# Kernel tuning notes

Hardware: AMD Instinct MI355X
Metric: run time of the kernel (lower is better)

Reference implementation:

```python
import jax, jax.numpy as jnp
import numpy as np

L, D, A = 3, 128, 64
NREL2 = 2 * 200 + 1
N_NODE, N_EDGE = 100000, 600000
NQ, N_ENT = 512, 50000


def setup_inputs() -> dict:
    key = jax.random.key(0)
    ks = jax.random.split(key, 30)
    s = 0.05
    inp = {
        "rela_embed": jax.random.normal(ks[0], (L, NREL2, D)) * s,
        "Ws": jax.random.normal(ks[1], (L, A, D)) * s,
        "Wr": jax.random.normal(ks[2], (L, A, D)) * s,
        "Wqr_w": jax.random.normal(ks[3], (L, A, D)) * s,
        "Wqr_b": jax.random.normal(ks[4], (L, A)) * s,
        "Wtau": jax.random.normal(ks[5], (L, A, D)) * s,
        "walpha_w": jax.random.normal(ks[6], (L, 1, A)) * s,
        "walpha_b": jax.random.normal(ks[7], (L, 1)) * s,
        "Wh": jax.random.normal(ks[8], (L, D, D)) * s,
        "wt1": jax.random.normal(ks[9], (L, 1, D)) * s,
        "bt1": jax.random.normal(ks[10], (L, 1, D)) * s,
        "wt2": jax.random.normal(ks[11], (L, 1, D)) * s,
        "bt2": jax.random.normal(ks[12], (L, 1, D)) * s,
        "Wih": jax.random.normal(ks[13], (L, 3 * D, D)) * s,
        "Whh": jax.random.normal(ks[14], (L, 3 * D, D)) * s,
        "bih": jax.random.normal(ks[15], (L, 3 * D)) * s,
        "bhh": jax.random.normal(ks[16], (L, 3 * D)) * s,
        "Wfinal": jax.random.normal(ks[17], (D,)) * s,
        "q_rel": jax.random.randint(ks[18], (NQ,), 0, NREL2),
        "q_tau": jax.random.randint(ks[19], (NQ,), 0, 366),
        "edge_ridx": jax.random.randint(ks[20], (L, N_EDGE), 0, NQ),
        "edge_rel": jax.random.randint(ks[21], (L, N_EDGE), 0, NREL2),
        "edge_tau": jax.random.randint(ks[22], (L, N_EDGE), 0, 366),
        "edge_sub": jax.random.randint(ks[23], (L, N_EDGE), 0, N_NODE),
        "edge_obj": jax.random.randint(ks[24], (L, N_EDGE), 0, N_NODE),
        "nodes_batch": jax.random.randint(ks[25], (N_NODE,), 0, NQ),
        "nodes_ent": jax.random.randint(ks[26], (N_NODE,), 0, N_ENT),
        "n_ent": N_ENT,
    }
    return inp


def _gru_cell(x, h, Wih, Whh, bih, bhh):
    # PyTorch GRU cell semantics (seq_len == 1)
    gi = x @ Wih.T + bih  # [N, 3D]
    gh = h @ Whh.T + bhh
    i_r, i_z, i_n = jnp.split(gi, 3, axis=-1)
    h_r, h_z, h_n = jnp.split(gh, 3, axis=-1)
    r = jax.nn.sigmoid(i_r + h_r)
    z = jax.nn.sigmoid(i_z + h_z)
    n = jnp.tanh(i_n + r * h_n)
    return (1.0 - z) * n + z * h


def reference(rela_embed, Ws, Wr, Wqr_w, Wqr_b, Wtau, walpha_w, walpha_b, Wh,
              wt1, bt1, wt2, bt2, Wih, Whh, bih, bhh, Wfinal,
              q_rel, q_tau, edge_ridx, edge_rel, edge_tau, edge_sub, edge_obj,
              nodes_batch, nodes_ent, n_ent):
    n_node = nodes_batch.shape[0]
    nq = q_rel.shape[0]
    d = Wh.shape[-1]
    hidden = jnp.zeros((n_node, d), dtype=rela_embed.dtype)
    h0 = jnp.zeros((n_node, d), dtype=rela_embed.dtype)
    coe_timediff = 0.2  # computed in original but unused downstream

    for l in range(rela_embed.shape[0]):
        sub, rel, obj = edge_sub[l], edge_rel[l], edge_obj[l]
        ridx = edge_ridx[l]
        hs = hidden[sub]                      # [E, D] gather
        hr = rela_embed[l][rel]               # [E, D] embedding gather
        h_qr = rela_embed[l][q_rel][ridx]     # [E, D]
        taus_q = q_tau[ridx]
        tau = jnp.where(edge_tau[l] >= 0, edge_tau[l], taus_q)
        delta = (tau - taus_q).astype(rela_embed.dtype)[:, None]  # [E, 1]
        h_hau = wt1[l] * delta + bt1[l] + jnp.sin(wt2[l] * delta + bt2[l])
        message = hs + hr + h_hau
        attn = jax.nn.relu(hs @ Ws[l].T + hr @ Wr[l].T + h_qr @ Wqr_w[l].T
                           + Wqr_b[l] + h_hau @ Wtau[l].T)  # [E, A]
        alpha = jax.nn.sigmoid(attn @ walpha_w[l].T + walpha_b[l])  # [E, 1]
        msg = alpha * message
        agg = jax.ops.segment_sum(msg, obj, num_segments=n_node)  # scatter-add
        hidden = jax.nn.relu(agg @ Wh[l].T)
        # old_nodes_new_idx == identity here, so index_copy of h0 is passthrough
        h = _gru_cell(hidden, h0, Wih[l], Whh[l], bih[l], bhh[l])
        hidden, h0 = h, h

    scores = hidden @ Wfinal  # [n_node]
    scores_all = jnp.zeros((nq, n_ent), dtype=scores.dtype)
    scores_all = scores_all.at[nodes_batch, nodes_ent].set(scores)
    return scores_all
```

## Files before the change

kernel.cpp:

```cpp
#include <hip/hip_runtime.h>
#include <hip/hip_bf16.h>
#include <math.h>

typedef __hip_bfloat16 bf16;
typedef __attribute__((ext_vector_type(8))) short s8v;
typedef __attribute__((ext_vector_type(4))) float f4v;
typedef __attribute__((ext_vector_type(4))) float f4x;
typedef __attribute__((ext_vector_type(4))) short s4v;

constexpr int Lc = 3, Dc = 128, Ac = 64, NREL2c = 401;
constexpr int NEc = 600000, NNc = 100000, NQc = 512, NENTc = 50000;
constexpr int NTAUc = 731;
constexpr int HBITS = 18;
constexpr unsigned HSIZE = 1u << HBITS, HMASK = HSIZE - 1u;
constexpr int NBLK = (NNc + 255) / 256;
constexpr int NTILE = 4;

constexpr float SFX = 32767.f, SFXI = 1.f / 32767.f;

constexpr int O_RELA = 0;
constexpr int O_WS   = O_RELA + Lc * NREL2c * Dc;
constexpr int O_WR   = O_WS   + Lc * Ac * Dc;
constexpr int O_WQRW = O_WR   + Lc * Ac * Dc;
constexpr int O_WQRB = O_WQRW + Lc * Ac * Dc;
constexpr int O_WTAU = O_WQRB + Lc * Ac;
constexpr int O_WAW  = O_WTAU + Lc * Ac * Dc;
constexpr int O_WAB  = O_WAW  + Lc * Ac;
constexpr int O_WH   = O_WAB  + Lc;
constexpr int O_WT1  = O_WH   + Lc * Dc * Dc;
constexpr int O_BT1  = O_WT1  + Lc * Dc;
constexpr int O_WT2  = O_BT1  + Lc * Dc;
constexpr int O_BT2  = O_WT2  + Lc * Dc;
constexpr int O_WIH  = O_BT2  + Lc * Dc;
constexpr int O_WHH  = O_WIH  + Lc * 3 * Dc * Dc;
constexpr int O_BIH  = O_WHH  + Lc * 3 * Dc * Dc;
constexpr int O_BHH  = O_BIH  + Lc * 3 * Dc;
constexpr int O_WF   = O_BHH  + Lc * 3 * Dc;
constexpr int NWTAB  = O_WF + Dc;

__device__ const int KOFF[19] = {O_RELA, O_WS, O_WR, O_WQRW, O_WQRB, O_WTAU, O_WAW,
                                 O_WAB, O_WH, O_WT1, O_BT1, O_WT2, O_BT2, O_WIH,
                                 O_WHH, O_BIH, O_BHH, O_WF, NWTAB};

struct Ptrs { const void* p[18]; };

__device__ __forceinline__ float b2f(bf16 x) { return __bfloat162float(x); }
__device__ __forceinline__ float bsf(unsigned short u) {
  return __uint_as_float((unsigned)u << 16);
}
__device__ __forceinline__ float sigm(float x) { return 1.f / (1.f + expf(-x)); }
__device__ __forceinline__ float s2f(short s) { return (float)s * SFXI; }
__device__ __forceinline__ short f2s(float v) { return (short)__float2int_rn(v * SFX); }
__device__ __forceinline__ unsigned short f2b(float v) {
  bf16 h = __float2bfloat16(v);
  return *(unsigned short*)&h;
}
__device__ __forceinline__ f4v mfma16(s8v a, s8v b, f4v c) {
  return __builtin_amdgcn_mfma_f32_16x16x32_bf16(a, b, c, 0, 0, 0);
}

__global__ void detect_dtype(const unsigned* __restrict__ w, int* __restrict__ flag) {
  int lane = threadIdx.x & 63;
  int cnt = 0;
  for (int k = lane; k < 256; k += 64) {
    unsigned e = (w[k] >> 7) & 0xffu;
    cnt += (e >= 96u && e <= 140u) ? 1 : 0;
  }
#pragma unroll
  for (int o = 32; o; o >>= 1) cnt += __shfl_xor(cnt, o, 64);
  if (lane == 0) *flag = (cnt >= 128) ? 0 : 1;
}

__global__ void convert_weights(Ptrs ps, const int* __restrict__ flag,
                                unsigned short* __restrict__ wtab) {
  int idx = blockIdx.x * 256 + threadIdx.x;
  if (idx >= NWTAB) return;
  int b = 0;
  while (idx >= KOFF[b + 1]) ++b;
  int j = idx - KOFF[b];
  unsigned short v;
  if (*flag) v = f2b(((const float*)ps.p[b])[j]);
  else v = ((const unsigned short*)ps.p[b])[j];
  wtab[idx] = v;
}

__global__ void prep_hhau(int l, const bf16* __restrict__ W, float* __restrict__ Hh) {
  int idx = blockIdx.x * 256 + threadIdx.x;
  if (idx >= NTAUc * Dc) return;
  int t = idx >> 7, d = idx & 127;
  float delta = (float)(t - 365);
  Hh[idx] = b2f(W[O_WT1 + l * Dc + d]) * delta + b2f(W[O_BT1 + l * Dc + d]) +
            sinf(b2f(W[O_WT2 + l * Dc + d]) * delta + b2f(W[O_BT2 + l * Dc + d]));
}

__global__ void prep_yr(int l, const bf16* __restrict__ W, float* __restrict__ Yr) {
  int idx = blockIdx.x * 256 + threadIdx.x;
  if (idx >= NREL2c * Ac) return;
  int r = idx >> 6, a = idx & 63;
  const bf16* x = W + O_RELA + (size_t)(l * NREL2c + r) * Dc;
  const bf16* w = W + O_WR + (size_t)(l * Ac + a) * Dc;
  float s = 0.f;
  for (int d = 0; d < Dc; ++d) s = fmaf(b2f(x[d]), b2f(w[d]), s);
  Yr[idx] = s;
}

__global__ void prep_yqr(int l, const bf16* __restrict__ W, const int* __restrict__ q_rel,
                         float* __restrict__ Yqr) {
  int idx = blockIdx.x * 256 + threadIdx.x;
  if (idx >= NQc * Ac) return;
  int q = idx >> 6, a = idx & 63;
  const bf16* x = W + O_RELA + (size_t)(l * NREL2c + q_rel[q]) * Dc;
  const bf16* w = W + O_WQRW + (size_t)(l * Ac + a) * Dc;
  float s = b2f(W[O_WQRB + l * Ac + a]);
  for (int d = 0; d < Dc; ++d) s = fmaf(b2f(x[d]), b2f(w[d]), s);
  Yqr[idx] = s;
}

__global__ void prep_yh(int l, const float* __restrict__ Hh, const bf16* __restrict__ W,
                        float* __restrict__ Yh) {
  int idx = blockIdx.x * 256 + threadIdx.x;
  if (idx >= NTAUc * Ac) return;
  int t = idx >> 6, a = idx & 63;
  const float* x = Hh + (size_t)t * Dc;
  const bf16* w = W + O_WTAU + (size_t)(l * Ac + a) * Dc;
  float s = 0.f;
  for (int d = 0; d < Dc; ++d) s = fmaf(x[d], b2f(w[d]), s);
  Yh[idx] = s;
}

__global__ void k_count(const int* __restrict__ e_obj, int base, int* __restrict__ cnt) {
  int e = blockIdx.x * 256 + threadIdx.x;
  if (e < NEc) atomicAdd(&cnt[e_obj[base + e]], 1);
}

__global__ void k_scan1(const int* __restrict__ cnt, int* __restrict__ bsum) {
  __shared__ int s[256];
  int t = threadIdx.x, g = blockIdx.x * 256 + t;
  s[t] = g < NNc ? cnt[g] : 0;
  __syncthreads();
  for (int o = 128; o > 0; o >>= 1) {
    if (t < o) s[t] += s[t + o];
    __syncthreads();
  }
  if (t == 0) bsum[blockIdx.x] = s[0];
}

__global__ void k_scan2(const int* __restrict__ bsum, int* __restrict__ bpre,
                        int* __restrict__ offsets) {
  if (threadIdx.x == 0) {
    int run = 0;
    for (int i = 0; i < NBLK; ++i) { bpre[i] = run; run += bsum[i]; }
    offsets[NNc] = run;
  }
}

__global__ void k_scan3(const int* __restrict__ cnt, const int* __restrict__ bpre,
                        int* __restrict__ offsets, int* __restrict__ cursor) {
  __shared__ int s[256];
  int t = threadIdx.x, g = blockIdx.x * 256 + t;
  int c = g < NNc ? cnt[g] : 0;
  s[t] = c;
  __syncthreads();
  for (int o = 1; o < 256; o <<= 1) {
    int v = (t >= o) ? s[t - o] : 0;
    __syncthreads();
    s[t] += v;
    __syncthreads();
  }
  if (g < NNc) {
    int off = s[t] - c + bpre[blockIdx.x];
    offsets[g] = off;
    cursor[g] = off;
  }
}

__global__ void k_fill(const int* __restrict__ e_obj, int base, int* __restrict__ cursor,
                       int* __restrict__ eidx) {
  int e = blockIdx.x * 256 + threadIdx.x;
  if (e < NEc) {
    int pos = atomicAdd(&cursor[e_obj[base + e]], 1);
    eidx[pos] = e;
  }
}

__global__ __launch_bounds__(256, 2) void alpha_kernel(
    int l, const bf16* __restrict__ W, const int* __restrict__ e_sub,
    const int* __restrict__ e_rel, const int* __restrict__ e_ridx,
    const int* __restrict__ e_tau, const int* __restrict__ q_tau,
    const short* __restrict__ state, const float* __restrict__ Yr,
    const float* __restrict__ Yqr, const float* __restrict__ Yh,
    float* __restrict__ alphab, unsigned short* __restrict__ dixb) {
  const int tid = threadIdx.x, lane = tid & 63, w = tid >> 6;
  const int col = lane & 15, quad = lane >> 4;
  const unsigned short* Wu = (const unsigned short*)W;
  s8v Bf[4][4];
  if (l != 0) {
#pragma unroll
    for (int kt = 0; kt < 4; ++kt)
#pragma unroll
      for (int ct = 0; ct < 4; ++ct)
        Bf[kt][ct] =
            *(const s8v*)&Wu[O_WS + (size_t)(l * Ac + ct * 16 + col) * Dc + kt * 32 + quad * 8];
  }
  float wa[4];
#pragma unroll
  for (int ct = 0; ct < 4; ++ct) wa[ct] = b2f(W[O_WAW + l * Ac + ct * 16 + col]);
  const float wb = b2f(W[O_WAB + l]);
  const int base = l * NEc;
  const int gw0 = blockIdx.x * 4 + w, nw = gridDim.x * 4;
  for (int g = gw0; g < NEc / 16; g += nw) {
    int e0 = g * 16;
    int sub16 = e_sub[base + e0 + col];
    int rel16 = e_rel[base + e0 + col];
    int ridx16 = e_ridx[base + e0 + col];
    int et16 = e_tau[base + e0 + col];
    int tq16 = q_tau[ridx16];
    int dix16 = ((et16 >= 0) ? et16 : tq16) - tq16 + 365;
    if (lane < 16) dixb[e0 + lane] = (unsigned short)dix16;
    f4v acc[4];
#pragma unroll
    for (int ct = 0; ct < 4; ++ct) acc[ct] = (f4v)0.f;
    if (l != 0) {
#pragma unroll
      for (int kt = 0; kt < 4; ++kt) {
        const short* sp = &state[(size_t)sub16 * Dc + kt * 32 + quad * 8];
        s8v raw = *(const s8v*)sp;
        s8v a;
#pragma unroll
        for (int j = 0; j < 8; ++j) a[j] = (short)f2b((float)raw[j] * SFXI);
#pragma unroll
        for (int ct = 0; ct < 4; ++ct) acc[ct] = mfma16(a, Bf[kt][ct], acc[ct]);
      }
    }
    float sums[4];
#pragma unroll
    for (int r = 0; r < 4; ++r) {
      int m = quad * 4 + r;
      int rel_m = __shfl(rel16, m, 64);
      int ridx_m = __shfl(ridx16, m, 64);
      int dix_m = __shfl(dix16, m, 64);
      float s = 0.f;
#pragma unroll
      for (int ct = 0; ct < 4; ++ct) {
        int a = ct * 16 + col;
        float v = acc[ct][r] + Yr[rel_m * Ac + a] + Yqr[ridx_m * Ac + a] + Yh[dix_m * Ac + a];
        s = fmaf(fmaxf(v, 0.f), wa[ct], s);
      }
      s += __shfl_xor(s, 1, 64);
      s += __shfl_xor(s, 2, 64);
      s += __shfl_xor(s, 4, 64);
      s += __shfl_xor(s, 8, 64);
      sums[r] = s;
    }
    int rr = col - quad * 4;
    if (rr >= 0 && rr < 4) alphab[e0 + col] = sigm(sums[rr] + wb);
  }
}

__global__ __launch_bounds__(256) void gather_kernel(
    int l, const bf16* __restrict__ W, const int* __restrict__ offsets,
    const int* __restrict__ eidx, const float* __restrict__ alphab,
    const unsigned short* __restrict__ dixb, const int* __restrict__ e_sub,
    const int* __restrict__ e_rel, const short* __restrict__ state,
    const float* __restrict__ Hh, float* __restrict__ agg) {
  const int lane = threadIdx.x & 63;
  const int gw = (blockIdx.x * 256 + threadIdx.x) >> 6;
  const int nw = (gridDim.x * 256) >> 6;
  const int base = l * NEc;
  for (int i = gw; i < NNc; i += nw) {
    float a0 = 0.f, a1 = 0.f;
    int s = offsets[i], en = offsets[i + 1];
    for (int p = s; p < en; ++p) {
      int e = eidx[p];
      float al = alphab[e];
      int rel = e_rel[base + e];
      int dix = dixb[e];
      float hs0 = 0.f, hs1 = 0.f;
      if (l != 0) {
        int sub = e_sub[base + e];
        hs0 = s2f(state[(size_t)sub * Dc + lane]);
        hs1 = s2f(state[(size_t)sub * Dc + 64 + lane]);
      }
      const bf16* hrp = W + O_RELA + (size_t)(l * NREL2c + rel) * Dc;
      a0 = fmaf(al, hs0 + b2f(hrp[lane]) + Hh[dix * Dc + lane], a0);
      a1 = fmaf(al, hs1 + b2f(hrp[64 + lane]) + Hh[dix * Dc + 64 + lane], a1);
    }
    agg[(size_t)i * Dc + lane] = a0;
    agg[(size_t)i * Dc + 64 + lane] = a1;
  }
}

__global__ __launch_bounds__(256, 2) void node_update(
    int l, const bf16* __restrict__ W, const float* __restrict__ agg,
    short* __restrict__ state) {
  __shared__ __align__(16) unsigned short ldsAhi[64][136];
  __shared__ __align__(16) unsigned short ldsAlo[64][136];
  __shared__ __align__(16) unsigned short ldsH[64][136];
  const int tid = threadIdx.x;
  const int lane = tid & 63;
  const int w = tid >> 6;
  const int col = lane & 15;
  const int quad = lane >> 4;
  const int kb = quad * 8;
  const unsigned short* Wu = (const unsigned short*)W;

  s8v whb[2][4];
#pragma unroll
  for (int kt = 0; kt < 4; ++kt) {
    whb[0][kt] = *(const s8v*)&Wu[O_WH + (size_t)(l * Dc + w * 16 + col) * Dc + kt * 32 + kb];
    whb[1][kt] =
        *(const s8v*)&Wu[O_WH + (size_t)(l * Dc + (w + 4) * 16 + col) * Dc + kt * 32 + kb];
  }

#pragma unroll 1
  for (int tile = 0; tile < NTILE; ++tile) {
    const int n0 = (blockIdx.x * NTILE + tile) * 64;
    if (n0 >= NNc) break;
    if (tile) __syncthreads();
    for (int e = tid; e < 64 * 32; e += 256) {
      int i = e >> 5, c = (e & 31) * 4;
      int node = n0 + i;
      f4x av = (f4x)0.f;
      if (node < NNc) av = __builtin_nontemporal_load((const f4x*)&agg[(size_t)node * Dc + c]);
      s4v hi4, lo4;
#pragma unroll
      for (int j = 0; j < 4; ++j) {
        unsigned short hi = f2b(av[j]);
        hi4[j] = (short)hi;
        lo4[j] = (short)f2b(av[j] - bsf(hi));
      }
      *(s4v*)&ldsAhi[i][c] = hi4;
      *(s4v*)&ldsAlo[i][c] = lo4;
      if (l != 0) {
        s4v hv4 = (s4v)0, hb4;
        if (node < NNc) hv4 = *(const s4v*)&state[(size_t)node * Dc + c];
#pragma unroll
        for (int j = 0; j < 4; ++j) hb4[j] = (short)f2b(s2f(hv4[j]));
        *(s4v*)&ldsH[i][c] = hb4;
      }
    }
    __syncthreads();

    f4v xo[2][4];
#pragma unroll
    for (int c = 0; c < 2; ++c)
#pragma unroll
      for (int mt = 0; mt < 4; ++mt) xo[c][mt] = (f4v)0.f;
#pragma unroll
    for (int kt = 0; kt < 4; ++kt) {
      int ko = kt * 32 + kb;
#pragma unroll
      for (int mt = 0; mt < 4; ++mt) {
        s8v ahi = *(const s8v*)&ldsAhi[mt * 16 + col][ko];
        s8v alo = *(const s8v*)&ldsAlo[mt * 16 + col][ko];
        xo[0][mt] = mfma16(ahi, whb[0][kt], xo[0][mt]);
        xo[0][mt] = mfma16(alo, whb[0][kt], xo[0][mt]);
        xo[1][mt] = mfma16(ahi, whb[1][kt], xo[1][mt]);
        xo[1][mt] = mfma16(alo, whb[1][kt], xo[1][mt]);
      }
    }
    __syncthreads();
#pragma unroll
    for (int c = 0; c < 2; ++c) {
      int t = w + 4 * c;
#pragma unroll
      for (int mt = 0; mt < 4; ++mt) {
#pragma unroll
        for (int r = 0; r < 4; ++r) {
          float x = fmaxf(xo[c][mt][r], 0.f);
          unsigned short hi = f2b(x);
          ldsAhi[mt * 16 + quad * 4 + r][t * 16 + col] = hi;
          ldsAlo[mt * 16 + quad * 4 + r][t * 16 + col] = f2b(x - bsf(hi));
        }
      }
    }
    __syncthreads();

#pragma unroll 1
    for (int hs = 0; hs < 2; ++hs) {
      const int jcol = hs * 64 + w * 16 + col;
      const int R = l * 384 + jcol;
      f4v racc[4], zacc[4], niacc[4], nhacc[4];
#pragma unroll
      for (int mt = 0; mt < 4; ++mt) {
        racc[mt] = (f4v)0.f;
        zacc[mt] = (f4v)0.f;
        niacc[mt] = (f4v)0.f;
        nhacc[mt] = (f4v)0.f;
      }
#pragma unroll
      for (int kt = 0; kt < 4; ++kt) {
        int ko = kt * 32 + kb;
        s8v bir = *(const s8v*)&Wu[O_WIH + (size_t)R * Dc + ko];
        s8v biz = *(const s8v*)&Wu[O_WIH + (size_t)(R + 128) * Dc + ko];
        s8v bin = *(const s8v*)&Wu[O_WIH + (size_t)(R + 256) * Dc + ko];
#pragma unroll
        for (int mt = 0; mt < 4; ++mt) {
          s8v xhi = *(const s8v*)&ldsAhi[mt * 16 + col][ko];
          s8v xlo = *(const s8v*)&ldsAlo[mt * 16 + col][ko];
          racc[mt] = mfma16(xhi, bir, racc[mt]);
          racc[mt] = mfma16(xlo, bir, racc[mt]);
          zacc[mt] = mfma16(xhi, biz, zacc[mt]);
          zacc[mt] = mfma16(xlo, biz, zacc[mt]);
          niacc[mt] = mfma16(xhi, bin, niacc[mt]);
          niacc[mt] = mfma16(xlo, bin, niacc[mt]);
        }
        if (l != 0) {
          s8v bhr = *(const s8v*)&Wu[O_WHH + (size_t)R * Dc + ko];
          s8v bhz = *(const s8v*)&Wu[O_WHH + (size_t)(R + 128) * Dc + ko];
          s8v bhn = *(const s8v*)&Wu[O_WHH + (size_t)(R + 256) * Dc + ko];
#pragma unroll
          for (int mt = 0; mt < 4; ++mt) {
            s8v hf = *(const s8v*)&ldsH[mt * 16 + col][ko];
            racc[mt] = mfma16(hf, bhr, racc[mt]);
            zacc[mt] = mfma16(hf, bhz, zacc[mt]);
            nhacc[mt] = mfma16(hf, bhn, nhacc[mt]);
          }
        }
      }
      float bir_ = b2f(W[O_BIH + R]) + b2f(W[O_BHH + R]);
      float biz_ = b2f(W[O_BIH + R + 128]) + b2f(W[O_BHH + R + 128]);
      float bin_ = b2f(W[O_BIH + R + 256]);
      float bhn_ = b2f(W[O_BHH + R + 256]);
#pragma unroll
      for (int mt = 0; mt < 4; ++mt) {
#pragma unroll
        for (int r_ = 0; r_ < 4; ++r_) {
          int node = n0 + mt * 16 + quad * 4 + r_;
          if (node < NNc) {
            float rg = sigm(racc[mt][r_] + bir_);
            float zg = sigm(zacc[mt][r_] + biz_);
            float ng = tanhf(niacc[mt][r_] + bin_ + rg * (nhacc[mt][r_] + bhn_));
            size_t idx = (size_t)node * Dc + jcol;
            float h0 = (l != 0) ? s2f(state[idx]) : 0.f;
            __builtin_nontemporal_store(f2s((1.f - zg) * ng + zg * h0), &state[idx]);
          }
        }
      }
    }
  }
}

__global__ __launch_bounds__(256) void score_kernel(const short* __restrict__ state,
                                                    const bf16* __restrict__ W,
                                                    float* __restrict__ scores) {
  const int lane = threadIdx.x & 63;
  const int gw = (blockIdx.x * 256 + threadIdx.x) >> 6;
  const int nw = (gridDim.x * 256) >> 6;
  const float w0 = b2f(W[O_WF + lane]), w1 = b2f(W[O_WF + 64 + lane]);
  for (int i = gw; i < NNc; i += nw) {
    float v = s2f(state[(size_t)i * Dc + lane]) * w0 + s2f(state[(size_t)i * Dc + 64 + lane]) * w1;
#pragma unroll
    for (int o = 32; o; o >>= 1) v += __shfl_xor(v, o, 64);
    if (lane == 0) scores[i] = v;
  }
}

__global__ void zero_out(unsigned* __restrict__ out, const int* __restrict__ flag) {
  long words = ((long)NQc * NENTc / 2) * (*flag ? 2 : 1);
  long i = (long)blockIdx.x * 256 + threadIdx.x;
  long stride = (long)gridDim.x * 256;
  for (; i < words; i += stride) out[i] = 0u;
}

__device__ __forceinline__ unsigned hpos(unsigned pos) { return (pos * 2654435761u) >> (32 - HBITS); }

__global__ void scat1(const int* __restrict__ nb, const int* __restrict__ ne,
                      unsigned* __restrict__ hkey, int* __restrict__ hval) {
  int i = blockIdx.x * 256 + threadIdx.x;
  if (i >= NNc) return;
  unsigned pos = (unsigned)(nb[i] * NENTc + ne[i]);
  unsigned key = pos + 1u;
  unsigned h = hpos(pos);
  while (true) {
    unsigned prev = atomicCAS(&hkey[h], 0u, key);
    if (prev == 0u || prev == key) {
      atomicMax(&hval[h], i);
      break;
    }
    h = (h + 1u) & HMASK;
  }
}

__global__ void scat2(const int* __restrict__ nb, const int* __restrict__ ne,
                      const unsigned* __restrict__ hkey, const int* __restrict__ hval,
                      const float* __restrict__ scores, const int* __restrict__ flag,
                      void* __restrict__ out) {
  int i = blockIdx.x * 256 + threadIdx.x;
  if (i >= NNc) return;
  unsigned pos = (unsigned)(nb[i] * NENTc + ne[i]);
  unsigned key = pos + 1u;
  unsigned h = hpos(pos);
  while (true) {
    unsigned k = hkey[h];
    if (k == key) {
      if (hval[h] == i) {
        if (*flag) ((float*)out)[pos] = scores[i];
        else ((bf16*)out)[pos] = __float2bfloat16(scores[i]);
      }
      break;
    }
    if (k == 0u) break;
    h = (h + 1u) & HMASK;
  }
}

extern "C" void kernel_launch(void* const* d_in, const int* in_sizes, int n_in,
                              void* d_out, int out_size, void* d_ws, size_t ws_size,
                              hipStream_t stream) {
  const int* q_rel = (const int*)d_in[18];
  const int* q_tau = (const int*)d_in[19];
  const int* e_ridx = (const int*)d_in[20];
  const int* e_rel = (const int*)d_in[21];
  const int* e_tau = (const int*)d_in[22];
  const int* e_sub = (const int*)d_in[23];
  const int* e_obj = (const int*)d_in[24];
  const int* n_batch = (const int*)d_in[25];
  const int* n_ent_i = (const int*)d_in[26];

  char* p = (char*)d_ws;
  auto alloc = [&](size_t bytes) {
    void* r = (void*)p;
    p += (bytes + 255) & ~(size_t)255;
    return r;
  };
  int* flag = (int*)alloc(256);
  bf16* wtab = (bf16*)alloc((size_t)NWTAB * 2);
  short* state = (short*)alloc((size_t)NNc * Dc * 2);
  char* big = (char*)alloc((size_t)NNc * Dc * 2);
  float* Yr = (float*)big;
  float* Yqr = (float*)(big + 102912);
  float* Hh = (float*)(big + 233984);
  float* Yh = (float*)(big + 608256);
  float* alphab = (float*)(big + 800000);
  unsigned short* dixb = (unsigned short*)(big + 3200000);
  int* cnt = (int*)(big + 4400128);
  int* cursor = (int*)(big + 4800384);
  int* offsets = (int*)(big + 5200640);
  int* bsum = (int*)(big + 5600768);
  int* bpre = (int*)(big + 5602560);
  int* eidx = (int*)(big + 5604352);
  float* scores = (float*)big;
  unsigned* hkey = (unsigned*)(big + 400128);
  int* hval = (int*)(big + 400128 + (size_t)HSIZE * 4);

  float* agg = (float*)d_out;

  detect_dtype<<<1, 64, 0, stream>>>((const unsigned*)d_in[0], flag);
  Ptrs ps;
  for (int i = 0; i < 18; ++i) ps.p[i] = d_in[i];
  convert_weights<<<(NWTAB + 255) / 256, 256, 0, stream>>>(ps, flag, (unsigned short*)wtab);
  hipMemsetAsync(state, 0, (size_t)NNc * Dc * 2, stream);

  for (int l = 0; l < Lc; ++l) {
    hipMemsetAsync(cnt, 0, (size_t)NNc * 4, stream);
    prep_hhau<<<(NTAUc * Dc + 255) / 256, 256, 0, stream>>>(l, wtab, Hh);
    prep_yr<<<(NREL2c * Ac + 255) / 256, 256, 0, stream>>>(l, wtab, Yr);
    prep_yqr<<<(NQc * Ac + 255) / 256, 256, 0, stream>>>(l, wtab, q_rel, Yqr);
    prep_yh<<<(NTAUc * Ac + 255) / 256, 256, 0, stream>>>(l, Hh, wtab, Yh);
    k_count<<<(NEc + 255) / 256, 256, 0, stream>>>(e_obj, l * NEc, cnt);
    k_scan1<<<NBLK, 256, 0, stream>>>(cnt, bsum);
    k_scan2<<<1, 64, 0, stream>>>(bsum, bpre, offsets);
    k_scan3<<<NBLK, 256, 0, stream>>>(cnt, bpre, offsets, cursor);
    k_fill<<<(NEc + 255) / 256, 256, 0, stream>>>(e_obj, l * NEc, cursor, eidx);
    alpha_kernel<<<2048, 256, 0, stream>>>(l, wtab, e_sub, e_rel, e_ridx, e_tau, q_tau,
                                           state, Yr, Yqr, Yh, alphab, dixb);
    gather_kernel<<<2048, 256, 0, stream>>>(l, wtab, offsets, eidx, alphab, dixb, e_sub,
                                            e_rel, state, Hh, agg);
    node_update<<<(NNc + 64 * NTILE - 1) / (64 * NTILE), 256, 0, stream>>>(l, wtab, agg, state);
  }
  score_kernel<<<1024, 256, 0, stream>>>(state, wtab, scores);
  hipMemsetAsync(hkey, 0, (size_t)HSIZE * 4, stream);
  hipMemsetAsync(hval, 0, (size_t)HSIZE * 4, stream);
  zero_out<<<2048, 256, 0, stream>>>((unsigned*)d_out, flag);
  scat1<<<(NNc + 255) / 256, 256, 0, stream>>>(n_batch, n_ent_i, hkey, hval);
  scat2<<<(NNc + 255) / 256, 256, 0, stream>>>(n_batch, n_ent_i, hkey, hval, scores, flag, d_out);
}
```

Baseline: 1.892 ms.

## Stage GRU outputs in LDS for coalesced state writes and reuse cached h0

The GRU gate computation moves into a templated helper that returns results in registers. Outputs are staged through LDS and written to state as 16-byte coalesced rows, replacing scattered 2-byte nontemporal stores and the per-element global re-read of h0, which now comes from the raw fixed-point copy in LDS. Occupancy is raised to 3 blocks per SM and NTILE is halved. The costs are an extra conversion of the fixed-point h into bf16 inside the inner MFMA loop, two more barriers per tile, and higher register pressure under the tighter launch bound.

```diff
diff --git a/kernel.cpp b/kernel.cpp
--- a/kernel.cpp
+++ b/kernel.cpp
@@ -14,7 +14,7 @@
 constexpr int HBITS = 18;
 constexpr unsigned HSIZE = 1u << HBITS, HMASK = HSIZE - 1u;
 constexpr int NBLK = (NNc + 255) / 256;
-constexpr int NTILE = 4;
+constexpr int NTILE = 2;
 
 constexpr float SFX = 32767.f, SFXI = 1.f / 32767.f;
 
@@ -290,7 +290,73 @@
   }
 }
 
-__global__ __launch_bounds__(256, 2) void node_update(
+template <int HS>
+__device__ __forceinline__ void gate_half(
+    int l, const unsigned short* __restrict__ Wu, const bf16* __restrict__ W,
+    int w, int col, int quad, int kb, int n0,
+    unsigned short (&ldsAhi)[64][136], unsigned short (&ldsAlo)[64][136],
+    unsigned short (&ldsH)[64][136], float (&hout)[16]) {
+  const int jcol = HS * 64 + w * 16 + col;
+  const int R = l * 384 + jcol;
+  f4v racc[4], zacc[4], niacc[4], nhacc[4];
+#pragma unroll
+  for (int mt = 0; mt < 4; ++mt) {
+    racc[mt] = (f4v)0.f;
+    zacc[mt] = (f4v)0.f;
+    niacc[mt] = (f4v)0.f;
+    nhacc[mt] = (f4v)0.f;
+  }
+#pragma unroll
+  for (int kt = 0; kt < 4; ++kt) {
+    int ko = kt * 32 + kb;
+    s8v bir = *(const s8v*)&Wu[O_WIH + (size_t)R * Dc + ko];
+    s8v biz = *(const s8v*)&Wu[O_WIH + (size_t)(R + 128) * Dc + ko];
+    s8v bin = *(const s8v*)&Wu[O_WIH + (size_t)(R + 256) * Dc + ko];
+#pragma unroll
+    for (int mt = 0; mt < 4; ++mt) {
+      s8v xhi = *(const s8v*)&ldsAhi[mt * 16 + col][ko];
+      s8v xlo = *(const s8v*)&ldsAlo[mt * 16 + col][ko];
+      racc[mt] = mfma16(xhi, bir, racc[mt]);
+      racc[mt] = mfma16(xlo, bir, racc[mt]);
+      zacc[mt] = mfma16(xhi, biz, zacc[mt]);
+      zacc[mt] = mfma16(xlo, biz, zacc[mt]);
+      niacc[mt] = mfma16(xhi, bin, niacc[mt]);
+      niacc[mt] = mfma16(xlo, bin, niacc[mt]);
+    }
+    if (l != 0) {
+      s8v bhr = *(const s8v*)&Wu[O_WHH + (size_t)R * Dc + ko];
+      s8v bhz = *(const s8v*)&Wu[O_WHH + (size_t)(R + 128) * Dc + ko];
+      s8v bhn = *(const s8v*)&Wu[O_WHH + (size_t)(R + 256) * Dc + ko];
+#pragma unroll
+      for (int mt = 0; mt < 4; ++mt) {
+        s8v raw = *(const s8v*)&ldsH[mt * 16 + col][ko];
+        s8v hf;
+#pragma unroll
+        for (int j = 0; j < 8; ++j) hf[j] = (short)f2b((float)raw[j] * SFXI);
+        racc[mt] = mfma16(hf, bhr, racc[mt]);
+        zacc[mt] = mfma16(hf, bhz, zacc[mt]);
+        nhacc[mt] = mfma16(hf, bhn, nhacc[mt]);
+      }
+    }
+  }
+  float bir_ = b2f(W[O_BIH + R]) + b2f(W[O_BHH + R]);
+  float biz_ = b2f(W[O_BIH + R + 128]) + b2f(W[O_BHH + R + 128]);
+  float bin_ = b2f(W[O_BIH + R + 256]);
+  float bhn_ = b2f(W[O_BHH + R + 256]);
+#pragma unroll
+  for (int mt = 0; mt < 4; ++mt) {
+#pragma unroll
+    for (int r_ = 0; r_ < 4; ++r_) {
+      float rg = sigm(racc[mt][r_] + bir_);
+      float zg = sigm(zacc[mt][r_] + biz_);
+      float ng = tanhf(niacc[mt][r_] + bin_ + rg * (nhacc[mt][r_] + bhn_));
+      float h0 = (l != 0) ? s2f((short)ldsH[mt * 16 + quad * 4 + r_][jcol]) : 0.f;
+      hout[mt * 4 + r_] = (1.f - zg) * ng + zg * h0;
+    }
+  }
+}
+
+__global__ __launch_bounds__(256, 3) void node_update(
     int l, const bf16* __restrict__ W, const float* __restrict__ agg,
     short* __restrict__ state) {
   __shared__ __align__(16) unsigned short ldsAhi[64][136];
@@ -332,11 +398,9 @@
       *(s4v*)&ldsAhi[i][c] = hi4;
       *(s4v*)&ldsAlo[i][c] = lo4;
       if (l != 0) {
-        s4v hv4 = (s4v)0, hb4;
+        s4v hv4 = (s4v)0;
         if (node < NNc) hv4 = *(const s4v*)&state[(size_t)node * Dc + c];
-#pragma unroll
-        for (int j = 0; j < 4; ++j) hb4[j] = (short)f2b(s2f(hv4[j]));
-        *(s4v*)&ldsH[i][c] = hb4;
+        *(s4v*)&ldsH[i][c] = hv4;
       }
     }
     __syncthreads();
@@ -376,66 +440,26 @@
     }
     __syncthreads();
 
-#pragma unroll 1
-    for (int hs = 0; hs < 2; ++hs) {
-      const int jcol = hs * 64 + w * 16 + col;
-      const int R = l * 384 + jcol;
-      f4v racc[4], zacc[4], niacc[4], nhacc[4];
-#pragma unroll
-      for (int mt = 0; mt < 4; ++mt) {
-        racc[mt] = (f4v)0.f;
-        zacc[mt] = (f4v)0.f;
-        niacc[mt] = (f4v)0.f;
-        nhacc[mt] = (f4v)0.f;
-      }
-#pragma unroll
-      for (int kt = 0; kt < 4; ++kt) {
-        int ko = kt * 32 + kb;
-        s8v bir = *(const s8v*)&Wu[O_WIH + (size_t)R * Dc + ko];
-        s8v biz = *(const s8v*)&Wu[O_WIH + (size_t)(R + 128) * Dc + ko];
-        s8v bin = *(const s8v*)&Wu[O_WIH + (size_t)(R + 256) * Dc + ko];
-#pragma unroll
-        for (int mt = 0; mt < 4; ++mt) {
-          s8v xhi = *(const s8v*)&ldsAhi[mt * 16 + col][ko];
-          s8v xlo = *(const s8v*)&ldsAlo[mt * 16 + col][ko];
-          racc[mt] = mfma16(xhi, bir, racc[mt]);
-          racc[mt] = mfma16(xlo, bir, racc[mt]);
-          zacc[mt] = mfma16(xhi, biz, zacc[mt]);
-          zacc[mt] = mfma16(xlo, biz, zacc[mt]);
-          niacc[mt] = mfma16(xhi, bin, niacc[mt]);
-          niacc[mt] = mfma16(xlo, bin, niacc[mt]);
-        }
-        if (l != 0) {
-          s8v bhr = *(const s8v*)&Wu[O_WHH + (size_t)R * Dc + ko];
-          s8v bhz = *(const s8v*)&Wu[O_WHH + (size_t)(R + 128) * Dc + ko];
-          s8v bhn = *(const s8v*)&Wu[O_WHH + (size_t)(R + 256) * Dc + ko];
-#pragma unroll
-          for (int mt = 0; mt < 4; ++mt) {
-            s8v hf = *(const s8v*)&ldsH[mt * 16 + col][ko];
-            racc[mt] = mfma16(hf, bhr, racc[mt]);
-            zacc[mt] = mfma16(hf, bhz, zacc[mt]);
-            nhacc[mt] = mfma16(hf, bhn, nhacc[mt]);
-          }
-        }
-      }
-      float bir_ = b2f(W[O_BIH + R]) + b2f(W[O_BHH + R]);
-      float biz_ = b2f(W[O_BIH + R + 128]) + b2f(W[O_BHH + R + 128]);
-      float bin_ = b2f(W[O_BIH + R + 256]);
-      float bhn_ = b2f(W[O_BHH + R + 256]);
-#pragma unroll
-      for (int mt = 0; mt < 4; ++mt) {
-#pragma unroll
-        for (int r_ = 0; r_ < 4; ++r_) {
-          int node = n0 + mt * 16 + quad * 4 + r_;
-          if (node < NNc) {
-            float rg = sigm(racc[mt][r_] + bir_);
-            float zg = sigm(zacc[mt][r_] + biz_);
-            float ng = tanhf(niacc[mt][r_] + bin_ + rg * (nhacc[mt][r_] + bhn_));
-            size_t idx = (size_t)node * Dc + jcol;
-            float h0 = (l != 0) ? s2f(state[idx]) : 0.f;
-            __builtin_nontemporal_store(f2s((1.f - zg) * ng + zg * h0), &state[idx]);
-          }
-        }
+    float hout0[16], hout1[16];
+    gate_half<0>(l, Wu, W, w, col, quad, kb, n0, ldsAhi, ldsAlo, ldsH, hout0);
+    gate_half<1>(l, Wu, W, w, col, quad, kb, n0, ldsAhi, ldsAlo, ldsH, hout1);
+    __syncthreads();
+#pragma unroll
+    for (int mt = 0; mt < 4; ++mt) {
+#pragma unroll
+      for (int r_ = 0; r_ < 4; ++r_) {
+        int row = mt * 16 + quad * 4 + r_;
+        ldsAhi[row][w * 16 + col] = (unsigned short)f2s(hout0[mt * 4 + r_]);
+        ldsAhi[row][64 + w * 16 + col] = (unsigned short)f2s(hout1[mt * 4 + r_]);
+      }
+    }
+    __syncthreads();
+    for (int e = tid; e < 64 * 16; e += 256) {
+      int i = e >> 4, c = (e & 15) * 8;
+      int node = n0 + i;
+      if (node < NNc) {
+        s8v hv = *(const s8v*)&ldsAhi[i][c];
+        __builtin_nontemporal_store(hv, (s8v*)&state[(size_t)node * Dc + c]);
       }
     }
   }
```

Result: slower. 2.139 ms (+13.1%).
